# Optimization experiments

Measured on AMD Instinct MI355X. Metric: run time of the kernel, lower is better.

Reference implementation:

```python
import jax, jax.numpy as jnp
import numpy as np

D = 256
H = 8
DH = D // H
N = 100000
B = 256
T = 131072
HID_FUSE = 256   # fuse MLP hidden = d_model
HID_HEAD = 256   # QuantileHeads hidden
NQ = 3           # quantiles (q10, q50, q90)


def setup_inputs() -> dict:
    key = jax.random.key(0)
    ks = jax.random.split(key, 32)
    p = lambda k, *s: (0.02 * jax.random.normal(k, s, dtype=jnp.float32))
    inp = {
        'node_embeddings': jax.random.normal(ks[0], (N, D), dtype=jnp.float32),
        'target_index': jax.random.randint(ks[1], (B,), 0, N),
        'port_index': jax.random.randint(ks[2], (T,), 0, N),
        'port_batch': jnp.sort(jax.random.randint(ks[3], (T,), 0, B)),
        'port_weight': jax.random.uniform(ks[4], (T,), dtype=jnp.float32),
        # PMA pooling params (learnable seed + MHA projections, no biases)
        'seed': p(ks[5], D),
        'Wq_p': p(ks[6], D, D), 'Wk_p': p(ks[7], D, D), 'Wv_p': p(ks[8], D, D), 'Wo_p': p(ks[9], D, D),
        # target->portfolio cross-attention params
        'Wq_c': p(ks[10], D, D), 'Wk_c': p(ks[11], D, D), 'Wv_c': p(ks[12], D, D), 'Wo_c': p(ks[13], D, D),
        # fuse LayerNorm(3d) + MLP
        'ln_g': jnp.ones((3 * D,), jnp.float32), 'ln_b': jnp.zeros((3 * D,), jnp.float32),
        'fuse_W1': p(ks[14], 3 * D, HID_FUSE), 'fuse_b1': jnp.zeros((HID_FUSE,), jnp.float32),
        'fuse_W2': p(ks[15], HID_FUSE, D), 'fuse_b2': jnp.zeros((D,), jnp.float32),
        # quantile heads MLP
        'head_W1': p(ks[16], D, HID_HEAD), 'head_b1': jnp.zeros((HID_HEAD,), jnp.float32),
        'head_W2': p(ks[17], HID_HEAD, NQ), 'head_b2': jnp.zeros((NQ,), jnp.float32),
    }
    return inp


def _segment_attend(logits, v, seg, num_segments):
    # logits [T,H], v [T,H,DH], seg [T] -> pooled [num_segments, H, DH]
    m = jax.ops.segment_max(logits, seg, num_segments=num_segments)  # [B,H]
    e = jnp.exp(logits - m[seg])                                      # [T,H]
    s = jax.ops.segment_sum(e, seg, num_segments=num_segments)        # [B,H]
    p = e / (s[seg] + 1e-9)
    return jax.ops.segment_sum(p[..., None] * v, seg, num_segments=num_segments)


def reference(node_embeddings, target_index, port_index, port_batch, port_weight,
              seed, Wq_p, Wk_p, Wv_p, Wo_p, Wq_c, Wk_c, Wv_c, Wo_c,
              ln_g, ln_b, fuse_W1, fuse_b1, fuse_W2, fuse_b2,
              head_W1, head_b1, head_W2, head_b2):
    b = target_index.shape[0]
    scale = float(DH) ** -0.5
    tgt = node_embeddings[target_index]          # [B,D]
    tok = node_embeddings[port_index]            # [T,D]
    logw = jnp.log(port_weight + 1e-8)           # DV01 weighting as logit bias

    # --- PMA: learnable seed query pools DV01-weighted portfolio tokens ---
    q_p = (seed @ Wq_p).reshape(H, DH)
    k_p = (tok @ Wk_p).reshape(-1, H, DH)
    v_p = (tok @ Wv_p).reshape(-1, H, DH)
    lg_p = jnp.einsum('thd,hd->th', k_p, q_p) * scale + logw[:, None]
    pooled = _segment_attend(lg_p, v_p, port_batch, b).reshape(b, D)
    contexts = pooled @ Wo_p                     # [B,D]; zeros for empty portfolios

    # --- target -> portfolio cross-attention (residual) ---
    q_c = (tgt @ Wq_c).reshape(b, H, DH)
    k_c = (tok @ Wk_c).reshape(-1, H, DH)
    v_c = (tok @ Wv_c).reshape(-1, H, DH)
    lg_c = jnp.einsum('thd,thd->th', k_c, q_c[port_batch]) * scale + logw[:, None]
    att = _segment_attend(lg_c, v_c, port_batch, b).reshape(b, D)
    fused = tgt + att @ Wo_c                     # [B,D]; == tgt for empty portfolios

    # --- fuse: concat -> LN -> MLP ---
    z = jnp.concatenate([tgt, contexts, fused], axis=-1)  # [B,3D]
    mu = jnp.mean(z, axis=-1, keepdims=True)
    var = jnp.var(z, axis=-1, keepdims=True)
    z = (z - mu) * jax.lax.rsqrt(var + 1e-5) * ln_g + ln_b
    z = jax.nn.relu(z @ fuse_W1 + fuse_b1) @ fuse_W2 + fuse_b2  # [B,D]

    # --- quantile heads ---
    out = jax.nn.relu(z @ head_W1 + head_b1) @ head_W2 + head_b2  # [B,NQ]
    return out
```

## Files before the change

kernel.cpp:

```cpp
#include <hip/hip_runtime.h>
#include <hip/hip_bf16.h>

typedef __attribute__((ext_vector_type(8))) short short8;
typedef __attribute__((ext_vector_type(4))) float floatx4;

#define SCALE 0.17677669529663687f

__device__ __forceinline__ unsigned short f2bf(float f) {
  unsigned int x = __float_as_uint(f);
  x += 0x7fffu + ((x >> 16) & 1u);
  return (unsigned short)(x >> 16);
}
__device__ __forceinline__ float bf2f(unsigned short u) {
  return __uint_as_float(((unsigned int)u) << 16);
}

__device__ __forceinline__ short8 load_cvt8(const float* p) {
  floatx4 a = *(const floatx4*)p;
  floatx4 b = *(const floatx4*)(p + 4);
  short8 r;
  r[0] = (short)f2bf(a[0]); r[1] = (short)f2bf(a[1]);
  r[2] = (short)f2bf(a[2]); r[3] = (short)f2bf(a[3]);
  r[4] = (short)f2bf(b[0]); r[5] = (short)f2bf(b[1]);
  r[6] = (short)f2bf(b[2]); r[7] = (short)f2bf(b[3]);
  return r;
}

__device__ __forceinline__ float block_sum(float v, float* red) {
  #pragma unroll
  for (int off = 32; off >= 1; off >>= 1) v += __shfl_xor(v, off, 64);
  __syncthreads();
  if ((threadIdx.x & 63) == 0) red[threadIdx.x >> 6] = v;
  __syncthreads();
  return red[0] + red[1] + red[2] + red[3];
}

__global__ __launch_bounds__(256) void setup_kernel(
    const float* __restrict__ seed,
    const float* __restrict__ Wq_p,
    const float* __restrict__ Wk_p,
    const int* __restrict__ port_batch,
    unsigned short* __restrict__ u_p_t,
    int* __restrict__ seg_start, int T, int B)
{
  __shared__ float seed_l[256];
  __shared__ float q_p[256];
  int tid = threadIdx.x;
  seed_l[tid] = seed[tid];
  __syncthreads();
  float acc = 0.f;
  for (int d = 0; d < 256; ++d) acc += seed_l[d] * Wq_p[d * 256 + tid];
  q_p[tid] = acc;
  __syncthreads();
  float hs[8];
  #pragma unroll
  for (int h = 0; h < 8; ++h) hs[h] = 0.f;
  #pragma unroll
  for (int c = 0; c < 32; ++c) {
    floatx4 wa = *(const floatx4*)(Wk_p + (size_t)tid * 256 + c * 8);
    floatx4 wb = *(const floatx4*)(Wk_p + (size_t)tid * 256 + c * 8 + 4);
    const int h = c >> 2;
    #pragma unroll
    for (int j = 0; j < 4; ++j) hs[h] += wa[j] * q_p[c * 8 + j];
    #pragma unroll
    for (int j = 0; j < 4; ++j) hs[h] += wb[j] * q_p[c * 8 + 4 + j];
  }
  #pragma unroll
  for (int h = 0; h < 8; ++h) u_p_t[h * 256 + tid] = f2bf(hs[h]);
  for (int b = tid; b <= B; b += 256) {
    int lo = 0, hi = T;
    while (lo < hi) { int mid = (lo + hi) >> 1; if (port_batch[mid] < b) lo = mid + 1; else hi = mid; }
    seg_start[b] = lo;
  }
}

__global__ __launch_bounds__(256, 1) void main_kernel(
    const float* __restrict__ node,
    const int* __restrict__ tgt_idx,
    const int* __restrict__ port_index,
    const float* __restrict__ port_weight,
    const float* __restrict__ Wq_c,
    const float* __restrict__ Wk_c,
    const float* __restrict__ Wv_p,
    const float* __restrict__ Wo_p,
    const float* __restrict__ Wv_c,
    const float* __restrict__ Wo_c,
    const float* __restrict__ ln_g,
    const float* __restrict__ ln_b,
    const float* __restrict__ fuse_W1,
    const float* __restrict__ fuse_b1,
    const float* __restrict__ fuse_W2,
    const float* __restrict__ fuse_b2,
    const float* __restrict__ head_W1,
    const float* __restrict__ head_b1,
    const float* __restrict__ head_W2,
    const float* __restrict__ head_b2,
    const unsigned short* __restrict__ u_p_t,
    const int* __restrict__ seg_start,
    float* __restrict__ out, int T)
{
  __shared__ __align__(16) char ovl[33792];
  __shared__ __align__(16) unsigned short E_t[16 * 72];
  __shared__ __align__(16) unsigned short u_all[16 * 264];
  __shared__ float tgt_l[256];
  __shared__ float q_c_l[256];
  __shared__ float l_lds[16];
  __shared__ float red_l[4];

  unsigned short* tok_lds = (unsigned short*)ovl;
  float* s_lds    = (float*)ovl;
  float* pooled_l = (float*)(ovl + 16448);
  float* att_l    = (float*)(ovl + 17472);
  float* z_l      = (float*)(ovl + 18496);
  float* zn_l     = (float*)(ovl + 21568);
  float* h1_l     = (float*)(ovl + 24640);
  float* z2_l     = (float*)(ovl + 25664);
  float* hh_l     = (float*)(ovl + 26688);

  const int tid  = threadIdx.x;
  const int b    = blockIdx.x;
  const int lane = tid & 63;
  const int w    = tid >> 6;
  const int q    = lane >> 4;
  const int n    = lane & 15;

  const int tix = tgt_idx[b];
  tgt_l[tid] = node[(size_t)tix * 256 + tid];
  if (tid < 16) l_lds[tid] = 0.f;
  __syncthreads();
  {
    float acc = 0.f;
    for (int d = 0; d < 256; ++d) acc += tgt_l[d] * Wq_c[d * 256 + tid];
    q_c_l[tid] = acc;
  }
  __syncthreads();
  {
    const int cn = tid >> 5, ch = (tid & 31) * 8;
    *(short8*)(u_all + cn * 264 + ch) = *(const short8*)(u_p_t + cn * 256 + ch);
    float hs[8];
    #pragma unroll
    for (int h = 0; h < 8; ++h) hs[h] = 0.f;
    #pragma unroll
    for (int c = 0; c < 32; ++c) {
      floatx4 wa = *(const floatx4*)(Wk_c + (size_t)tid * 256 + c * 8);
      floatx4 wb = *(const floatx4*)(Wk_c + (size_t)tid * 256 + c * 8 + 4);
      const int h = c >> 2;
      #pragma unroll
      for (int j = 0; j < 4; ++j) hs[h] += wa[j] * q_c_l[c * 8 + j];
      #pragma unroll
      for (int j = 0; j < 4; ++j) hs[h] += wb[j] * q_c_l[c * 8 + 4 + j];
    }
    #pragma unroll
    for (int h = 0; h < 8; ++h) u_all[(8 + h) * 264 + tid] = f2bf(hs[h]);
  }
  __syncthreads();

  short8 ufrag[8];
  #pragma unroll
  for (int s = 0; s < 8; ++s)
    ufrag[s] = *(const short8*)(u_all + n * 264 + q * 8 + s * 32);

  const int start  = seg_start[b];
  const int end    = seg_start[b + 1];
  const int ntiles = (end - start + 63) >> 6;

  floatx4 sacc[4];
  #pragma unroll
  for (int nt = 0; nt < 4; ++nt) sacc[nt] = (floatx4){0.f, 0.f, 0.f, 0.f};

  short8 cur[8], nxt[8];
  float pwc[4], pwn[4];

  if (ntiles > 0) {
    int t = start + w * 16 + n; int tc = t < T ? t : T - 1;
    const float* rp = node + (size_t)port_index[tc] * 256 + q * 8;
    #pragma unroll
    for (int s = 0; s < 8; ++s) cur[s] = load_cvt8(rp + s * 32);
    #pragma unroll
    for (int r = 0; r < 4; ++r) { int tr = start + w * 16 + q * 4 + r; pwc[r] = port_weight[tr < T ? tr : T - 1]; }
  }

  for (int it = 0; it < ntiles; ++it) {
    const int tbase = start + it * 64;
    if (it + 1 < ntiles) {
      int t = tbase + 64 + w * 16 + n; int tc = t < T ? t : T - 1;
      const float* rp = node + (size_t)port_index[tc] * 256 + q * 8;
      #pragma unroll
      for (int s = 0; s < 8; ++s) nxt[s] = load_cvt8(rp + s * 32);
      #pragma unroll
      for (int r = 0; r < 4; ++r) { int tr = tbase + 64 + w * 16 + q * 4 + r; pwn[r] = port_weight[tr < T ? tr : T - 1]; }
    }
    floatx4 lacc = (floatx4){0.f, 0.f, 0.f, 0.f};
    #pragma unroll
    for (int s = 0; s < 8; ++s)
      lacc = __builtin_amdgcn_mfma_f32_16x16x32_bf16(cur[s], ufrag[s], lacc, 0, 0, 0);
    float lsum = 0.f;
    #pragma unroll
    for (int r = 0; r < 4; ++r) {
      const int tr = tbase + w * 16 + q * 4 + r;
      float e = 0.f;
      if (tr < end) {
        float lg = lacc[r] * SCALE + logf(pwc[r] + 1e-8f);
        e = __expf(lg);
      }
      unsigned short eb = f2bf(e);
      E_t[n * 72 + w * 16 + q * 4 + r] = eb;
      lsum += bf2f(eb);
    }
    lsum += __shfl_xor(lsum, 16, 64);
    lsum += __shfl_xor(lsum, 32, 64);
    if (lane < 16) atomicAdd(&l_lds[lane], lsum);
    #pragma unroll
    for (int s = 0; s < 8; ++s)
      *(short8*)(tok_lds + (w * 16 + n) * 264 + q * 8 + s * 32) = cur[s];
    __syncthreads();
    short8 ea0 = *(const short8*)(E_t + n * 72 + q * 8);
    short8 ea1 = *(const short8*)(E_t + n * 72 + 32 + q * 8);
    #pragma unroll
    for (int nt = 0; nt < 4; ++nt) {
      const int dcol = w * 64 + nt * 16 + n;
      short8 b0, b1;
      #pragma unroll
      for (int j = 0; j < 8; ++j) b0[j] = (short)tok_lds[(q * 8 + j) * 264 + dcol];
      #pragma unroll
      for (int j = 0; j < 8; ++j) b1[j] = (short)tok_lds[(32 + q * 8 + j) * 264 + dcol];
      sacc[nt] = __builtin_amdgcn_mfma_f32_16x16x32_bf16(ea0, b0, sacc[nt], 0, 0, 0);
      sacc[nt] = __builtin_amdgcn_mfma_f32_16x16x32_bf16(ea1, b1, sacc[nt], 0, 0, 0);
    }
    __syncthreads();
    #pragma unroll
    for (int s = 0; s < 8; ++s) cur[s] = nxt[s];
    #pragma unroll
    for (int r = 0; r < 4; ++r) pwc[r] = pwn[r];
  }

  {
    float inv[4];
    #pragma unroll
    for (int r = 0; r < 4; ++r) inv[r] = 1.0f / (l_lds[q * 4 + r] + 1e-9f);
    #pragma unroll
    for (int nt = 0; nt < 4; ++nt) {
      #pragma unroll
      for (int r = 0; r < 4; ++r)
        s_lds[(q * 4 + r) * 257 + w * 64 + nt * 16 + n] = sacc[nt][r] * inv[r];
    }
  }
  __syncthreads();
  {
    const int h = tid >> 5;
    float po = 0.f, ao = 0.f;
    for (int d = 0; d < 256; ++d) {
      po += s_lds[h * 257 + d]       * Wv_p[d * 256 + tid];
      ao += s_lds[(8 + h) * 257 + d] * Wv_c[d * 256 + tid];
    }
    pooled_l[tid] = po;
    att_l[tid] = ao;
  }
  __syncthreads();
  {
    float cx = 0.f, at2 = 0.f;
    for (int o = 0; o < 256; ++o) {
      cx  += pooled_l[o] * Wo_p[o * 256 + tid];
      at2 += att_l[o]    * Wo_c[o * 256 + tid];
    }
    const float tg = tgt_l[tid];
    z_l[tid]       = tg;
    z_l[256 + tid] = cx;
    z_l[512 + tid] = tg + at2;
  }
  __syncthreads();
  const float z0 = z_l[tid], z1 = z_l[256 + tid], z2v = z_l[512 + tid];
  const float mu = block_sum(z0 + z1 + z2v, red_l) * (1.0f / 768.0f);
  const float d0 = z0 - mu, d1 = z1 - mu, d2 = z2v - mu;
  const float var = block_sum(d0 * d0 + d1 * d1 + d2 * d2, red_l) * (1.0f / 768.0f);
  const float rstd = 1.0f / sqrtf(var + 1e-5f);
  zn_l[tid]       = d0 * rstd * ln_g[tid]       + ln_b[tid];
  zn_l[256 + tid] = d1 * rstd * ln_g[256 + tid] + ln_b[256 + tid];
  zn_l[512 + tid] = d2 * rstd * ln_g[512 + tid] + ln_b[512 + tid];
  __syncthreads();
  {
    float a1 = fuse_b1[tid];
    for (int i = 0; i < 768; ++i) a1 += zn_l[i] * fuse_W1[i * 256 + tid];
    h1_l[tid] = fmaxf(a1, 0.f);
  }
  __syncthreads();
  {
    float a2 = fuse_b2[tid];
    for (int i = 0; i < 256; ++i) a2 += h1_l[i] * fuse_W2[i * 256 + tid];
    z2_l[tid] = a2;
  }
  __syncthreads();
  {
    float a3 = head_b1[tid];
    for (int i = 0; i < 256; ++i) a3 += z2_l[i] * head_W1[i * 256 + tid];
    hh_l[tid] = fmaxf(a3, 0.f);
  }
  __syncthreads();
  #pragma unroll
  for (int q2 = 0; q2 < 3; ++q2) {
    float p = hh_l[tid] * head_W2[tid * 3 + q2];
    float tot = block_sum(p, red_l);
    if (tid == 0) out[b * 3 + q2] = tot + head_b2[q2];
  }
}

extern "C" void kernel_launch(void* const* d_in, const int* in_sizes, int n_in,
                              void* d_out, int out_size, void* d_ws, size_t ws_size,
                              hipStream_t stream) {
  const float* node        = (const float*)d_in[0];
  const int*   tgt_idx     = (const int*)d_in[1];
  const int*   port_index  = (const int*)d_in[2];
  const int*   port_batch  = (const int*)d_in[3];
  const float* port_weight = (const float*)d_in[4];
  const float* seed        = (const float*)d_in[5];
  const float* Wq_p = (const float*)d_in[6];
  const float* Wk_p = (const float*)d_in[7];
  const float* Wv_p = (const float*)d_in[8];
  const float* Wo_p = (const float*)d_in[9];
  const float* Wq_c = (const float*)d_in[10];
  const float* Wk_c = (const float*)d_in[11];
  const float* Wv_c = (const float*)d_in[12];
  const float* Wo_c = (const float*)d_in[13];
  const float* ln_g = (const float*)d_in[14];
  const float* ln_b = (const float*)d_in[15];
  const float* fuse_W1 = (const float*)d_in[16];
  const float* fuse_b1 = (const float*)d_in[17];
  const float* fuse_W2 = (const float*)d_in[18];
  const float* fuse_b2 = (const float*)d_in[19];
  const float* head_W1 = (const float*)d_in[20];
  const float* head_b1 = (const float*)d_in[21];
  const float* head_W2 = (const float*)d_in[22];
  const float* head_b2 = (const float*)d_in[23];

  const int B = in_sizes[1];
  const int T = in_sizes[2];

  unsigned short* u_p_t = (unsigned short*)d_ws;
  int* seg = (int*)((char*)d_ws + 4096);

  setup_kernel<<<1, 256, 0, stream>>>(seed, Wq_p, Wk_p, port_batch, u_p_t, seg, T, B);
  main_kernel<<<B, 256, 0, stream>>>(node, tgt_idx, port_index, port_weight,
      Wq_c, Wk_c, Wv_p, Wo_p, Wv_c, Wo_c, ln_g, ln_b,
      fuse_W1, fuse_b1, fuse_W2, fuse_b2, head_W1, head_b1, head_W2, head_b2,
      u_p_t, seg, (float*)d_out, T);
}
```

Baseline: 356.5 us.

## Split segment attention across blocks and move per-batch prep into separate kernels

Splits the single per-portfolio kernel into three stages. A B-block setup computes per-target query projections, an attention kernel splits each segment's token tiles across S blocks and writes partial sums to workspace slabs, and a finalize kernel reduces the slabs and runs the MLP tail. The tail matvecs now use float4 weight loads with a split-K reduction through LDS. The aim is to use more CUs than the 256 single blocks with occupancy 1, and to cut the long serial tail per block. The cost is extra launches and the global round trip for the partials.

```diff
diff --git a/kernel.cpp b/kernel.cpp
--- a/kernel.cpp
+++ b/kernel.cpp
@@ -35,52 +35,216 @@
   return red[0] + red[1] + red[2] + red[3];
 }
 
+__device__ __forceinline__ void matvec256(const float* __restrict__ W,
+                                          const float* act, float* outv,
+                                          float* red4, int tid) {
+  const int c4 = tid & 63, kg = tid >> 6, c0 = c4 * 4;
+  floatx4 acc = (floatx4){0.f, 0.f, 0.f, 0.f};
+  const float* Wp = W + (size_t)(kg * 64) * 256 + c0;
+  const float* ap = act + kg * 64;
+  #pragma unroll 8
+  for (int k = 0; k < 64; ++k) {
+    floatx4 wv = *(const floatx4*)(Wp + (size_t)k * 256);
+    float a = ap[k];
+    acc[0] += a * wv[0]; acc[1] += a * wv[1];
+    acc[2] += a * wv[2]; acc[3] += a * wv[3];
+  }
+  *(floatx4*)(red4 + kg * 256 + c0) = acc;
+  __syncthreads();
+  outv[tid] = red4[tid] + red4[256 + tid] + red4[512 + tid] + red4[768 + tid];
+  __syncthreads();
+}
+
 __global__ __launch_bounds__(256) void setup_kernel(
+    const float* __restrict__ node,
+    const int* __restrict__ tgt_idx,
+    const int* __restrict__ port_batch,
     const float* __restrict__ seed,
     const float* __restrict__ Wq_p,
     const float* __restrict__ Wk_p,
-    const int* __restrict__ port_batch,
+    const float* __restrict__ Wq_c,
+    const float* __restrict__ Wk_c,
     unsigned short* __restrict__ u_p_t,
-    int* __restrict__ seg_start, int T, int B)
+    unsigned short* __restrict__ u_c_all,
+    int* __restrict__ seg, int T, int B)
 {
-  __shared__ float seed_l[256];
-  __shared__ float q_p[256];
-  int tid = threadIdx.x;
-  seed_l[tid] = seed[tid];
-  __syncthreads();
-  float acc = 0.f;
-  for (int d = 0; d < 256; ++d) acc += seed_l[d] * Wq_p[d * 256 + tid];
-  q_p[tid] = acc;
-  __syncthreads();
-  float hs[8];
-  #pragma unroll
-  for (int h = 0; h < 8; ++h) hs[h] = 0.f;
-  #pragma unroll
-  for (int c = 0; c < 32; ++c) {
-    floatx4 wa = *(const floatx4*)(Wk_p + (size_t)tid * 256 + c * 8);
-    floatx4 wb = *(const floatx4*)(Wk_p + (size_t)tid * 256 + c * 8 + 4);
-    const int h = c >> 2;
-    #pragma unroll
-    for (int j = 0; j < 4; ++j) hs[h] += wa[j] * q_p[c * 8 + j];
-    #pragma unroll
-    for (int j = 0; j < 4; ++j) hs[h] += wb[j] * q_p[c * 8 + 4 + j];
-  }
-  #pragma unroll
-  for (int h = 0; h < 8; ++h) u_p_t[h * 256 + tid] = f2bf(hs[h]);
-  for (int b = tid; b <= B; b += 256) {
+  __shared__ float act_l[256];
+  __shared__ float q_l[256];
+  __shared__ __align__(16) float red4[1024];
+  const int tid = threadIdx.x;
+  const int b = blockIdx.x;
+
+  if (tid == 0 || (tid == 64 && b == B - 1)) {
+    int key = (tid == 0) ? b : B;
     int lo = 0, hi = T;
-    while (lo < hi) { int mid = (lo + hi) >> 1; if (port_batch[mid] < b) lo = mid + 1; else hi = mid; }
-    seg_start[b] = lo;
-  }
-}
-
-__global__ __launch_bounds__(256, 1) void main_kernel(
+    while (lo < hi) { int mid = (lo + hi) >> 1; if (port_batch[mid] < key) lo = mid + 1; else hi = mid; }
+    seg[key] = lo;
+  }
+
+  act_l[tid] = node[(size_t)tgt_idx[b] * 256 + tid];
+  __syncthreads();
+  matvec256(Wq_c, act_l, q_l, red4, tid);
+
+  {
+    float hs[8];
+    #pragma unroll
+    for (int h = 0; h < 8; ++h) hs[h] = 0.f;
+    #pragma unroll
+    for (int c = 0; c < 32; ++c) {
+      floatx4 wa = *(const floatx4*)(Wk_c + (size_t)tid * 256 + c * 8);
+      floatx4 wb = *(const floatx4*)(Wk_c + (size_t)tid * 256 + c * 8 + 4);
+      const int h = c >> 2;
+      #pragma unroll
+      for (int j = 0; j < 4; ++j) hs[h] += wa[j] * q_l[c * 8 + j];
+      #pragma unroll
+      for (int j = 0; j < 4; ++j) hs[h] += wb[j] * q_l[c * 8 + 4 + j];
+    }
+    #pragma unroll
+    for (int h = 0; h < 8; ++h)
+      u_c_all[(size_t)b * 2048 + h * 256 + tid] = f2bf(hs[h]);
+  }
+
+  if (b == 0) {
+    __syncthreads();
+    act_l[tid] = seed[tid];
+    __syncthreads();
+    matvec256(Wq_p, act_l, q_l, red4, tid);
+    float hs[8];
+    #pragma unroll
+    for (int h = 0; h < 8; ++h) hs[h] = 0.f;
+    #pragma unroll
+    for (int c = 0; c < 32; ++c) {
+      floatx4 wa = *(const floatx4*)(Wk_p + (size_t)tid * 256 + c * 8);
+      floatx4 wb = *(const floatx4*)(Wk_p + (size_t)tid * 256 + c * 8 + 4);
+      const int h = c >> 2;
+      #pragma unroll
+      for (int j = 0; j < 4; ++j) hs[h] += wa[j] * q_l[c * 8 + j];
+      #pragma unroll
+      for (int j = 0; j < 4; ++j) hs[h] += wb[j] * q_l[c * 8 + 4 + j];
+    }
+    #pragma unroll
+    for (int h = 0; h < 8; ++h) u_p_t[h * 256 + tid] = f2bf(hs[h]);
+  }
+}
+
+__global__ __launch_bounds__(256, 3) void attn_kernel(
+    const float* __restrict__ node,
+    const int* __restrict__ port_index,
+    const float* __restrict__ port_weight,
+    const unsigned short* __restrict__ u_p_t,
+    const unsigned short* __restrict__ u_c_all,
+    const int* __restrict__ seg,
+    float* __restrict__ slabs, int T, int S)
+{
+  __shared__ __align__(16) unsigned short tok_lds[64 * 264];
+  __shared__ __align__(16) unsigned short E_t[16 * 72];
+  __shared__ float l_lds[16];
+
+  const int tid  = threadIdx.x;
+  const int s    = blockIdx.x;
+  const int b    = blockIdx.y;
+  const int lane = tid & 63;
+  const int w    = tid >> 6;
+  const int q    = lane >> 4;
+  const int n    = lane & 15;
+
+  if (tid < 16) l_lds[tid] = 0.f;
+
+  short8 ufrag[8];
+  const unsigned short* ubase = (n < 8) ? (u_p_t + n * 256)
+                                        : (u_c_all + (size_t)b * 2048 + (n - 8) * 256);
+  #pragma unroll
+  for (int s8 = 0; s8 < 8; ++s8)
+    ufrag[s8] = *(const short8*)(ubase + q * 8 + s8 * 32);
+
+  const int start  = seg[b];
+  const int end    = seg[b + 1];
+  const int ntiles = (end - start + 63) >> 6;
+
+  floatx4 sacc[4];
+  #pragma unroll
+  for (int nt = 0; nt < 4; ++nt) sacc[nt] = (floatx4){0.f, 0.f, 0.f, 0.f};
+
+  short8 cur[8], nxt[8];
+  float pwc[4], pwn[4];
+
+  __syncthreads();
+
+  if (s < ntiles) {
+    int t = start + s * 64 + w * 16 + n; int tc = t < T ? t : T - 1;
+    const float* rp = node + (size_t)port_index[tc] * 256 + q * 8;
+    #pragma unroll
+    for (int k = 0; k < 8; ++k) cur[k] = load_cvt8(rp + k * 32);
+    #pragma unroll
+    for (int r = 0; r < 4; ++r) { int tr = start + s * 64 + w * 16 + q * 4 + r; pwc[r] = port_weight[tr < T ? tr : T - 1]; }
+  }
+
+  for (int it = s; it < ntiles; it += S) {
+    const int tbase = start + it * 64;
+    if (it + S < ntiles) {
+      int t = start + (it + S) * 64 + w * 16 + n; int tc = t < T ? t : T - 1;
+      const float* rp = node + (size_t)port_index[tc] * 256 + q * 8;
+      #pragma unroll
+      for (int k = 0; k < 8; ++k) nxt[k] = load_cvt8(rp + k * 32);
+      #pragma unroll
+      for (int r = 0; r < 4; ++r) { int tr = start + (it + S) * 64 + w * 16 + q * 4 + r; pwn[r] = port_weight[tr < T ? tr : T - 1]; }
+    }
+    floatx4 lacc = (floatx4){0.f, 0.f, 0.f, 0.f};
+    #pragma unroll
+    for (int k = 0; k < 8; ++k)
+      lacc = __builtin_amdgcn_mfma_f32_16x16x32_bf16(cur[k], ufrag[k], lacc, 0, 0, 0);
+    float lsum = 0.f;
+    #pragma unroll
+    for (int r = 0; r < 4; ++r) {
+      const int tr = tbase + w * 16 + q * 4 + r;
+      float e = 0.f;
+      if (tr < end) {
+        float lg = lacc[r] * SCALE + logf(pwc[r] + 1e-8f);
+        e = __expf(lg);
+      }
+      unsigned short eb = f2bf(e);
+      E_t[n * 72 + w * 16 + q * 4 + r] = eb;
+      lsum += bf2f(eb);
+    }
+    lsum += __shfl_xor(lsum, 16, 64);
+    lsum += __shfl_xor(lsum, 32, 64);
+    if (lane < 16) atomicAdd(&l_lds[lane], lsum);
+    #pragma unroll
+    for (int k = 0; k < 8; ++k)
+      *(short8*)(tok_lds + (w * 16 + n) * 264 + q * 8 + k * 32) = cur[k];
+    __syncthreads();
+    short8 ea0 = *(const short8*)(E_t + n * 72 + q * 8);
+    short8 ea1 = *(const short8*)(E_t + n * 72 + 32 + q * 8);
+    #pragma unroll
+    for (int nt = 0; nt < 4; ++nt) {
+      const int dcol = w * 64 + nt * 16 + n;
+      short8 b0, b1;
+      #pragma unroll
+      for (int j = 0; j < 8; ++j) b0[j] = (short)tok_lds[(q * 8 + j) * 264 + dcol];
+      #pragma unroll
+      for (int j = 0; j < 8; ++j) b1[j] = (short)tok_lds[(32 + q * 8 + j) * 264 + dcol];
+      sacc[nt] = __builtin_amdgcn_mfma_f32_16x16x32_bf16(ea0, b0, sacc[nt], 0, 0, 0);
+      sacc[nt] = __builtin_amdgcn_mfma_f32_16x16x32_bf16(ea1, b1, sacc[nt], 0, 0, 0);
+    }
+    __syncthreads();
+    #pragma unroll
+    for (int k = 0; k < 8; ++k) cur[k] = nxt[k];
+    #pragma unroll
+    for (int r = 0; r < 4; ++r) pwc[r] = pwn[r];
+  }
+
+  float* sl = slabs + ((size_t)b * S + s) * 4224;
+  #pragma unroll
+  for (int nt = 0; nt < 4; ++nt)
+    #pragma unroll
+    for (int r = 0; r < 4; ++r)
+      sl[(q * 4 + r) * 256 + w * 64 + nt * 16 + n] = sacc[nt][r];
+  if (tid < 16) sl[4096 + tid] = l_lds[tid];
+}
+
+__global__ __launch_bounds__(256) void finalize_kernel(
     const float* __restrict__ node,
     const int* __restrict__ tgt_idx,
-    const int* __restrict__ port_index,
-    const float* __restrict__ port_weight,
-    const float* __restrict__ Wq_c,
-    const float* __restrict__ Wk_c,
     const float* __restrict__ Wv_p,
     const float* __restrict__ Wo_p,
     const float* __restrict__ Wv_c,
@@ -95,210 +259,126 @@
     const float* __restrict__ head_b1,
     const float* __restrict__ head_W2,
     const float* __restrict__ head_b2,
-    const unsigned short* __restrict__ u_p_t,
-    const int* __restrict__ seg_start,
-    float* __restrict__ out, int T)
+    const float* __restrict__ slabs,
+    float* __restrict__ out, int S)
 {
-  __shared__ __align__(16) char ovl[33792];
-  __shared__ __align__(16) unsigned short E_t[16 * 72];
-  __shared__ __align__(16) unsigned short u_all[16 * 264];
+  __shared__ float s_lds[16 * 257];
   __shared__ float tgt_l[256];
-  __shared__ float q_c_l[256];
-  __shared__ float l_lds[16];
+  __shared__ float va[256], vb[256];
+  __shared__ float z_l[768], zn_l[768];
+  __shared__ __align__(16) float red4[1024];
   __shared__ float red_l[4];
-
-  unsigned short* tok_lds = (unsigned short*)ovl;
-  float* s_lds    = (float*)ovl;
-  float* pooled_l = (float*)(ovl + 16448);
-  float* att_l    = (float*)(ovl + 17472);
-  float* z_l      = (float*)(ovl + 18496);
-  float* zn_l     = (float*)(ovl + 21568);
-  float* h1_l     = (float*)(ovl + 24640);
-  float* z2_l     = (float*)(ovl + 25664);
-  float* hh_l     = (float*)(ovl + 26688);
-
-  const int tid  = threadIdx.x;
-  const int b    = blockIdx.x;
-  const int lane = tid & 63;
-  const int w    = tid >> 6;
-  const int q    = lane >> 4;
-  const int n    = lane & 15;
-
-  const int tix = tgt_idx[b];
-  tgt_l[tid] = node[(size_t)tix * 256 + tid];
-  if (tid < 16) l_lds[tid] = 0.f;
-  __syncthreads();
-  {
-    float acc = 0.f;
-    for (int d = 0; d < 256; ++d) acc += tgt_l[d] * Wq_c[d * 256 + tid];
-    q_c_l[tid] = acc;
-  }
-  __syncthreads();
-  {
-    const int cn = tid >> 5, ch = (tid & 31) * 8;
-    *(short8*)(u_all + cn * 264 + ch) = *(const short8*)(u_p_t + cn * 256 + ch);
-    float hs[8];
-    #pragma unroll
-    for (int h = 0; h < 8; ++h) hs[h] = 0.f;
-    #pragma unroll
-    for (int c = 0; c < 32; ++c) {
-      floatx4 wa = *(const floatx4*)(Wk_c + (size_t)tid * 256 + c * 8);
-      floatx4 wb = *(const floatx4*)(Wk_c + (size_t)tid * 256 + c * 8 + 4);
-      const int h = c >> 2;
-      #pragma unroll
-      for (int j = 0; j < 4; ++j) hs[h] += wa[j] * q_c_l[c * 8 + j];
-      #pragma unroll
-      for (int j = 0; j < 4; ++j) hs[h] += wb[j] * q_c_l[c * 8 + 4 + j];
-    }
-    #pragma unroll
-    for (int h = 0; h < 8; ++h) u_all[(8 + h) * 264 + tid] = f2bf(hs[h]);
-  }
-  __syncthreads();
-
-  short8 ufrag[8];
-  #pragma unroll
-  for (int s = 0; s < 8; ++s)
-    ufrag[s] = *(const short8*)(u_all + n * 264 + q * 8 + s * 32);
-
-  const int start  = seg_start[b];
-  const int end    = seg_start[b + 1];
-  const int ntiles = (end - start + 63) >> 6;
-
-  floatx4 sacc[4];
-  #pragma unroll
-  for (int nt = 0; nt < 4; ++nt) sacc[nt] = (floatx4){0.f, 0.f, 0.f, 0.f};
-
-  short8 cur[8], nxt[8];
-  float pwc[4], pwn[4];
-
-  if (ntiles > 0) {
-    int t = start + w * 16 + n; int tc = t < T ? t : T - 1;
-    const float* rp = node + (size_t)port_index[tc] * 256 + q * 8;
-    #pragma unroll
-    for (int s = 0; s < 8; ++s) cur[s] = load_cvt8(rp + s * 32);
-    #pragma unroll
-    for (int r = 0; r < 4; ++r) { int tr = start + w * 16 + q * 4 + r; pwc[r] = port_weight[tr < T ? tr : T - 1]; }
-  }
-
-  for (int it = 0; it < ntiles; ++it) {
-    const int tbase = start + it * 64;
-    if (it + 1 < ntiles) {
-      int t = tbase + 64 + w * 16 + n; int tc = t < T ? t : T - 1;
-      const float* rp = node + (size_t)port_index[tc] * 256 + q * 8;
-      #pragma unroll
-      for (int s = 0; s < 8; ++s) nxt[s] = load_cvt8(rp + s * 32);
-      #pragma unroll
-      for (int r = 0; r < 4; ++r) { int tr = tbase + 64 + w * 16 + q * 4 + r; pwn[r] = port_weight[tr < T ? tr : T - 1]; }
-    }
-    floatx4 lacc = (floatx4){0.f, 0.f, 0.f, 0.f};
-    #pragma unroll
-    for (int s = 0; s < 8; ++s)
-      lacc = __builtin_amdgcn_mfma_f32_16x16x32_bf16(cur[s], ufrag[s], lacc, 0, 0, 0);
-    float lsum = 0.f;
-    #pragma unroll
-    for (int r = 0; r < 4; ++r) {
-      const int tr = tbase + w * 16 + q * 4 + r;
-      float e = 0.f;
-      if (tr < end) {
-        float lg = lacc[r] * SCALE + logf(pwc[r] + 1e-8f);
-        e = __expf(lg);
-      }
-      unsigned short eb = f2bf(e);
-      E_t[n * 72 + w * 16 + q * 4 + r] = eb;
-      lsum += bf2f(eb);
-    }
-    lsum += __shfl_xor(lsum, 16, 64);
-    lsum += __shfl_xor(lsum, 32, 64);
-    if (lane < 16) atomicAdd(&l_lds[lane], lsum);
-    #pragma unroll
-    for (int s = 0; s < 8; ++s)
-      *(short8*)(tok_lds + (w * 16 + n) * 264 + q * 8 + s * 32) = cur[s];
-    __syncthreads();
-    short8 ea0 = *(const short8*)(E_t + n * 72 + q * 8);
-    short8 ea1 = *(const short8*)(E_t + n * 72 + 32 + q * 8);
-    #pragma unroll
-    for (int nt = 0; nt < 4; ++nt) {
-      const int dcol = w * 64 + nt * 16 + n;
-      short8 b0, b1;
-      #pragma unroll
-      for (int j = 0; j < 8; ++j) b0[j] = (short)tok_lds[(q * 8 + j) * 264 + dcol];
-      #pragma unroll
-      for (int j = 0; j < 8; ++j) b1[j] = (short)tok_lds[(32 + q * 8 + j) * 264 + dcol];
-      sacc[nt] = __builtin_amdgcn_mfma_f32_16x16x32_bf16(ea0, b0, sacc[nt], 0, 0, 0);
-      sacc[nt] = __builtin_amdgcn_mfma_f32_16x16x32_bf16(ea1, b1, sacc[nt], 0, 0, 0);
-    }
-    __syncthreads();
-    #pragma unroll
-    for (int s = 0; s < 8; ++s) cur[s] = nxt[s];
-    #pragma unroll
-    for (int r = 0; r < 4; ++r) pwc[r] = pwn[r];
-  }
-
-  {
-    float inv[4];
-    #pragma unroll
-    for (int r = 0; r < 4; ++r) inv[r] = 1.0f / (l_lds[q * 4 + r] + 1e-9f);
-    #pragma unroll
-    for (int nt = 0; nt < 4; ++nt) {
-      #pragma unroll
-      for (int r = 0; r < 4; ++r)
-        s_lds[(q * 4 + r) * 257 + w * 64 + nt * 16 + n] = sacc[nt][r] * inv[r];
-    }
-  }
-  __syncthreads();
-  {
-    const int h = tid >> 5;
-    float po = 0.f, ao = 0.f;
-    for (int d = 0; d < 256; ++d) {
-      po += s_lds[h * 257 + d]       * Wv_p[d * 256 + tid];
-      ao += s_lds[(8 + h) * 257 + d] * Wv_c[d * 256 + tid];
-    }
-    pooled_l[tid] = po;
-    att_l[tid] = ao;
-  }
-  __syncthreads();
-  {
-    float cx = 0.f, at2 = 0.f;
-    for (int o = 0; o < 256; ++o) {
-      cx  += pooled_l[o] * Wo_p[o * 256 + tid];
-      at2 += att_l[o]    * Wo_c[o * 256 + tid];
-    }
+  __shared__ float l_loc[16];
+
+  const int tid = threadIdx.x;
+  const int b   = blockIdx.x;
+  const int c4 = tid & 63, kg = tid >> 6, c0 = c4 * 4;
+
+  const float* sb = slabs + (size_t)b * S * 4224;
+  for (int i = tid; i < 4096; i += 256) {
+    float v = 0.f;
+    for (int s = 0; s < S; ++s) v += sb[s * 4224 + i];
+    s_lds[(i >> 8) * 257 + (i & 255)] = v;
+  }
+  if (tid < 16) {
+    float v = 0.f;
+    for (int s = 0; s < S; ++s) v += sb[s * 4224 + 4096 + tid];
+    l_loc[tid] = v;
+  }
+  tgt_l[tid] = node[(size_t)tgt_idx[b] * 256 + tid];
+  __syncthreads();
+  #pragma unroll
+  for (int r = 0; r < 16; ++r)
+    s_lds[r * 257 + tid] *= 1.0f / (l_loc[r] + 1e-9f);
+  __syncthreads();
+
+  {
+    const int hrow = c0 >> 5;
+    floatx4 accP = (floatx4){0.f,0.f,0.f,0.f}, accA = accP;
+    const float* wp = Wv_p + (size_t)(kg * 64) * 256 + c0;
+    const float* wc = Wv_c + (size_t)(kg * 64) * 256 + c0;
+    const float* ap = s_lds + hrow * 257 + kg * 64;
+    const float* aa = s_lds + (8 + hrow) * 257 + kg * 64;
+    #pragma unroll 8
+    for (int k = 0; k < 64; ++k) {
+      floatx4 w1 = *(const floatx4*)(wp + (size_t)k * 256);
+      floatx4 w2 = *(const floatx4*)(wc + (size_t)k * 256);
+      float a1 = ap[k], a2 = aa[k];
+      accP[0] += a1*w1[0]; accP[1] += a1*w1[1]; accP[2] += a1*w1[2]; accP[3] += a1*w1[3];
+      accA[0] += a2*w2[0]; accA[1] += a2*w2[1]; accA[2] += a2*w2[2]; accA[3] += a2*w2[3];
+    }
+    *(floatx4*)(red4 + kg * 256 + c0) = accP;
+    __syncthreads();
+    float po = red4[tid] + red4[256 + tid] + red4[512 + tid] + red4[768 + tid];
+    __syncthreads();
+    *(floatx4*)(red4 + kg * 256 + c0) = accA;
+    __syncthreads();
+    float ao = red4[tid] + red4[256 + tid] + red4[512 + tid] + red4[768 + tid];
+    va[tid] = po; vb[tid] = ao;
+    __syncthreads();
+  }
+  {
+    floatx4 accP = (floatx4){0.f,0.f,0.f,0.f}, accA = accP;
+    const float* wp = Wo_p + (size_t)(kg * 64) * 256 + c0;
+    const float* wc = Wo_c + (size_t)(kg * 64) * 256 + c0;
+    #pragma unroll 8
+    for (int k = 0; k < 64; ++k) {
+      floatx4 w1 = *(const floatx4*)(wp + (size_t)k * 256);
+      floatx4 w2 = *(const floatx4*)(wc + (size_t)k * 256);
+      float a1 = va[kg * 64 + k], a2 = vb[kg * 64 + k];
+      accP[0] += a1*w1[0]; accP[1] += a1*w1[1]; accP[2] += a1*w1[2]; accP[3] += a1*w1[3];
+      accA[0] += a2*w2[0]; accA[1] += a2*w2[1]; accA[2] += a2*w2[2]; accA[3] += a2*w2[3];
+    }
+    *(floatx4*)(red4 + kg * 256 + c0) = accP;
+    __syncthreads();
+    float cx = red4[tid] + red4[256 + tid] + red4[512 + tid] + red4[768 + tid];
+    __syncthreads();
+    *(floatx4*)(red4 + kg * 256 + c0) = accA;
+    __syncthreads();
+    float at2 = red4[tid] + red4[256 + tid] + red4[512 + tid] + red4[768 + tid];
     const float tg = tgt_l[tid];
-    z_l[tid]       = tg;
-    z_l[256 + tid] = cx;
-    z_l[512 + tid] = tg + at2;
-  }
-  __syncthreads();
-  const float z0 = z_l[tid], z1 = z_l[256 + tid], z2v = z_l[512 + tid];
-  const float mu = block_sum(z0 + z1 + z2v, red_l) * (1.0f / 768.0f);
-  const float d0 = z0 - mu, d1 = z1 - mu, d2 = z2v - mu;
-  const float var = block_sum(d0 * d0 + d1 * d1 + d2 * d2, red_l) * (1.0f / 768.0f);
-  const float rstd = 1.0f / sqrtf(var + 1e-5f);
-  zn_l[tid]       = d0 * rstd * ln_g[tid]       + ln_b[tid];
-  zn_l[256 + tid] = d1 * rstd * ln_g[256 + tid] + ln_b[256 + tid];
-  zn_l[512 + tid] = d2 * rstd * ln_g[512 + tid] + ln_b[512 + tid];
-  __syncthreads();
-  {
-    float a1 = fuse_b1[tid];
-    for (int i = 0; i < 768; ++i) a1 += zn_l[i] * fuse_W1[i * 256 + tid];
-    h1_l[tid] = fmaxf(a1, 0.f);
-  }
-  __syncthreads();
-  {
-    float a2 = fuse_b2[tid];
-    for (int i = 0; i < 256; ++i) a2 += h1_l[i] * fuse_W2[i * 256 + tid];
-    z2_l[tid] = a2;
-  }
-  __syncthreads();
-  {
-    float a3 = head_b1[tid];
-    for (int i = 0; i < 256; ++i) a3 += z2_l[i] * head_W1[i * 256 + tid];
-    hh_l[tid] = fmaxf(a3, 0.f);
-  }
-  __syncthreads();
+    z_l[tid] = tg; z_l[256 + tid] = cx; z_l[512 + tid] = tg + at2;
+    __syncthreads();
+  }
+  {
+    const float z0 = z_l[tid], z1 = z_l[256 + tid], z2v = z_l[512 + tid];
+    const float mu = block_sum(z0 + z1 + z2v, red_l) * (1.0f / 768.0f);
+    const float d0 = z0 - mu, d1 = z1 - mu, d2 = z2v - mu;
+    const float var = block_sum(d0 * d0 + d1 * d1 + d2 * d2, red_l) * (1.0f / 768.0f);
+    const float rstd = 1.0f / sqrtf(var + 1e-5f);
+    zn_l[tid]       = d0 * rstd * ln_g[tid]       + ln_b[tid];
+    zn_l[256 + tid] = d1 * rstd * ln_g[256 + tid] + ln_b[256 + tid];
+    zn_l[512 + tid] = d2 * rstd * ln_g[512 + tid] + ln_b[512 + tid];
+    __syncthreads();
+  }
+  {
+    floatx4 acc = (floatx4){0.f,0.f,0.f,0.f};
+    const float* wp = fuse_W1 + (size_t)(kg * 192) * 256 + c0;
+    const float* ap = zn_l + kg * 192;
+    #pragma unroll 8
+    for (int k = 0; k < 192; ++k) {
+      floatx4 wv = *(const floatx4*)(wp + (size_t)k * 256);
+      float a = ap[k];
+      acc[0] += a*wv[0]; acc[1] += a*wv[1]; acc[2] += a*wv[2]; acc[3] += a*wv[3];
+    }
+    *(floatx4*)(red4 + kg * 256 + c0) = acc;
+    __syncthreads();
+    va[tid] = fmaxf(red4[tid] + red4[256 + tid] + red4[512 + tid] + red4[768 + tid] + fuse_b1[tid], 0.f);
+    __syncthreads();
+  }
+  matvec256(fuse_W2, va, vb, red4, tid);
+  {
+    vb[tid] += fuse_b2[tid];
+    __syncthreads();
+  }
+  matvec256(head_W1, vb, va, red4, tid);
+  {
+    va[tid] = fmaxf(va[tid] + head_b1[tid], 0.f);
+    __syncthreads();
+  }
   #pragma unroll
   for (int q2 = 0; q2 < 3; ++q2) {
-    float p = hh_l[tid] * head_W2[tid * 3 + q2];
+    float p = va[tid] * head_W2[tid * 3 + q2];
     float tot = block_sum(p, red_l);
     if (tid == 0) out[b * 3 + q2] = tot + head_b2[q2];
   }
@@ -335,12 +415,22 @@
   const int B = in_sizes[1];
   const int T = in_sizes[2];
 
-  unsigned short* u_p_t = (unsigned short*)d_ws;
-  int* seg = (int*)((char*)d_ws + 4096);
-
-  setup_kernel<<<1, 256, 0, stream>>>(seed, Wq_p, Wk_p, port_batch, u_p_t, seg, T, B);
-  main_kernel<<<B, 256, 0, stream>>>(node, tgt_idx, port_index, port_weight,
-      Wq_c, Wk_c, Wv_p, Wo_p, Wv_c, Wo_c, ln_g, ln_b,
+  unsigned short* u_p_t   = (unsigned short*)d_ws;
+  int*            seg     = (int*)((char*)d_ws + 4096);
+  unsigned short* u_c_all = (unsigned short*)((char*)d_ws + 8192);
+  size_t slab_off = 8192 + (size_t)B * 4096;
+  float* slabs = (float*)((char*)d_ws + slab_off);
+  size_t per_split = (size_t)B * 4224 * 4;
+  int S = 1;
+  if (ws_size >= slab_off + 4 * per_split) S = 4;
+  else if (ws_size >= slab_off + 2 * per_split) S = 2;
+
+  setup_kernel<<<B, 256, 0, stream>>>(node, tgt_idx, port_batch, seed,
+      Wq_p, Wk_p, Wq_c, Wk_c, u_p_t, u_c_all, seg, T, B);
+  attn_kernel<<<dim3(S, B), 256, 0, stream>>>(node, port_index, port_weight,
+      u_p_t, u_c_all, seg, slabs, T, S);
+  finalize_kernel<<<B, 256, 0, stream>>>(node, tgt_idx,
+      Wv_p, Wo_p, Wv_c, Wo_c, ln_g, ln_b,
       fuse_W1, fuse_b1, fuse_W2, fuse_b2, head_W1, head_b1, head_W2, head_b2,
-      u_p_t, seg, (float*)d_out, T);
-}
+      slabs, (float*)d_out, S);
+}
```

Result: faster. 320.7 us (-10.0%).
